# Optimization experiments

Hardware: AMD Instinct MI355X
Metric: run time of the kernel (lower is better)

Reference implementation:

```python
import jax, jax.numpy as jnp
import numpy as np

B, T, C = 2, 2048, 1024
N_HEAD = 16
BAND_WIDTH = 256

def setup_inputs() -> dict:
    key = jax.random.key(0)
    ks = jax.random.split(key, 5)
    s = 1.0 / np.sqrt(C)
    return {
        "x": jax.random.normal(ks[0], (B, T, C), dtype=jnp.float32),
        "Wq": jax.random.normal(ks[1], (C, C), dtype=jnp.float32) * s,
        "bq": jnp.zeros((C,), dtype=jnp.float32),
        "Wk": jax.random.normal(ks[2], (C, C), dtype=jnp.float32) * s,
        "bk": jnp.zeros((C,), dtype=jnp.float32),
        "Wv": jax.random.normal(ks[3], (C, C), dtype=jnp.float32) * s,
        "bv": jnp.zeros((C,), dtype=jnp.float32),
        "Wp": jax.random.normal(ks[4], (C, C), dtype=jnp.float32) * s,
        "bp": jnp.zeros((C,), dtype=jnp.float32),
    }

def _band_mask(t):
    # allowed: j <= i (causal) and j >= i - band_width (band)
    i = jnp.arange(t)[:, None]
    j = jnp.arange(t)[None, :]
    return (j <= i) & (j >= i - BAND_WIDTH)

def reference(x, Wq, bq, Wk, bk, Wv, bv, Wp, bp):
    b, t, c = x.shape
    hd = c // N_HEAD
    # projections -> [b, h, t, hd]
    def heads(w, bias):
        y = x @ w.T + bias
        return y.reshape(b, t, N_HEAD, hd).transpose(0, 2, 1, 3)
    q = heads(Wq, bq)
    k = heads(Wk, bk)
    v = heads(Wv, bv)
    scale = 1.0 / np.sqrt(hd)
    att = jnp.einsum('bhqd,bhkd->bhqk', q, k) * scale  # [b,h,t,t]
    mask = _band_mask(t)
    att = jnp.where(mask[None, None], att, -jnp.inf)
    att = jax.nn.softmax(att, axis=-1)
    y = jnp.einsum('bhqk,bhkd->bhqd', att, v)
    y = y.transpose(0, 2, 1, 3).reshape(b, t, c)
    return y @ Wp.T + bp
```

## Files before the change

kernel.cpp:

```cpp
#include <hip/hip_runtime.h>


typedef __attribute__((ext_vector_type(8))) short bf16x8;
typedef __attribute__((ext_vector_type(8))) unsigned short u16x8;
typedef __attribute__((ext_vector_type(4))) float f32x4;

__device__ __forceinline__ float bf2f(unsigned short u) {
  union { unsigned u; float f; } x; x.u = ((unsigned)u) << 16; return x.f;
}
__device__ __forceinline__ unsigned short f2bf(float f) {
  union { float f; unsigned u; } x; x.f = f;
  unsigned r = x.u + 0x7FFFu + ((x.u >> 16) & 1u);
  return (unsigned short)(r >> 16);
}

#define GLOAD_LDS16(g, l)                                                     \
  __builtin_amdgcn_global_load_lds(                                           \
      (__attribute__((address_space(1))) void*)(g),                           \
      (__attribute__((address_space(3))) void*)(l), 16, 0, 0)

__global__ void cvt_all(const float* __restrict__ x, const float* __restrict__ Wq,
                        const float* __restrict__ Wk, const float* __restrict__ Wv,
                        const float* __restrict__ Wp, unsigned short* __restrict__ xb,
                        unsigned short* __restrict__ wqkv,
                        unsigned short* __restrict__ wpb) {
  int i = blockIdx.x * 256 + threadIdx.x;
  const float* src;
  unsigned short* dst;
  int off;
  if (i < 1048576)      { src = x;  dst = xb;             off = i; }
  else if (i < 1310720) { src = Wq; dst = wqkv;           off = i - 1048576; }
  else if (i < 1572864) { src = Wk; dst = wqkv + 1048576; off = i - 1310720; }
  else if (i < 1835008) { src = Wv; dst = wqkv + 2097152; off = i - 1572864; }
  else                  { src = Wp; dst = wpb;            off = i - 1835008; }
  float4 v = ((const float4*)src)[off];
  ushort4 o;
  o.x = f2bf(v.x); o.y = f2bf(v.y); o.z = f2bf(v.z); o.w = f2bf(v.w);
  ((ushort4*)dst)[off] = o;
}

__global__ __launch_bounds__(256) void gemm_qkv(
    const unsigned short* __restrict__ A, const unsigned short* __restrict__ Wall,
    const float* __restrict__ b0, const float* __restrict__ b1,
    const float* __restrict__ b2, unsigned short* __restrict__ outp) {
  constexpr int K = 1024;
  __shared__ __align__(16) unsigned short As[128 * 32];
  __shared__ __align__(16) unsigned short Bs[128 * 32];
  int tid = threadIdx.x;
  int m0 = blockIdx.x * 128;
  int proj = blockIdx.y >> 3;
  int n0 = (blockIdx.y & 7) * 128;
  const unsigned short* W = Wall + (size_t)proj * (K * 1024);
  const float* bias = (proj == 0) ? b0 : ((proj == 1) ? b1 : b2);
  unsigned short* out = outp + (size_t)proj * 4194304;
  int w = tid >> 6, lane = tid & 63;
  int wm = (w >> 1) * 64, wn = (w & 1) * 64;
  int lm = lane & 15, quad = lane >> 4;

  f32x4 acc[4][4];
#pragma unroll
  for (int mi = 0; mi < 4; ++mi)
#pragma unroll
    for (int ni = 0; ni < 4; ++ni) acc[mi][ni] = (f32x4){0.f, 0.f, 0.f, 0.f};

  int o0 = tid * 16, o1 = o0 + 4096;
  int r0 = o0 >> 6, cb0 = o0 & 63;
  int r1 = o1 >> 6, cb1 = o1 & 63;
  const char* a0 = (const char*)A + (size_t)(m0 + r0) * (K * 2) + cb0;
  const char* a1 = (const char*)A + (size_t)(m0 + r1) * (K * 2) + cb1;
  const char* w0 = (const char*)W + (size_t)(n0 + r0) * (K * 2) + cb0;
  const char* w1 = (const char*)W + (size_t)(n0 + r1) * (K * 2) + cb1;
  char* lA = (char*)As;
  char* lB = (char*)Bs;

  for (int k0 = 0; k0 < K; k0 += 32) {
    GLOAD_LDS16(a0 + k0 * 2, lA + o0);
    GLOAD_LDS16(a1 + k0 * 2, lA + o1);
    GLOAD_LDS16(w0 + k0 * 2, lB + o0);
    GLOAD_LDS16(w1 + k0 * 2, lB + o1);
    __syncthreads();
    bf16x8 af[4], bfv[4];
#pragma unroll
    for (int mi = 0; mi < 4; ++mi)
      af[mi] = *(const bf16x8*)(As + (wm + mi * 16 + lm) * 32 + quad * 8);
#pragma unroll
    for (int ni = 0; ni < 4; ++ni)
      bfv[ni] = *(const bf16x8*)(Bs + (wn + ni * 16 + lm) * 32 + quad * 8);
#pragma unroll
    for (int mi = 0; mi < 4; ++mi)
#pragma unroll
      for (int ni = 0; ni < 4; ++ni)
        acc[mi][ni] = __builtin_amdgcn_mfma_f32_16x16x32_bf16(
            af[mi], bfv[ni], acc[mi][ni], 0, 0, 0);
    __syncthreads();
  }
#pragma unroll
  for (int mi = 0; mi < 4; ++mi) {
#pragma unroll
    for (int ni = 0; ni < 4; ++ni) {
      int gn = n0 + wn + ni * 16 + lm;
      float bv = bias[gn];
#pragma unroll
      for (int r = 0; r < 4; ++r) {
        int gm = m0 + wm + mi * 16 + quad * 4 + r;
        float val = acc[mi][ni][r] + bv;
        int bb = gm >> 11, tt = gm & 2047;
        int hh = gn >> 6, dd = gn & 63;
        size_t idx;
        if (proj == 2)
          idx = (((size_t)bb * 16 + hh) * 64 + dd) * 2048 + tt;
        else
          idx = (((size_t)bb * 16 + hh) * 2048 + tt) * 64 + dd;
        out[idx] = f2bf(val);
      }
    }
  }
}

__global__ __launch_bounds__(256) void gemm_p64(
    const unsigned short* __restrict__ A, const unsigned short* __restrict__ W,
    const float* __restrict__ bias, float* __restrict__ out) {
  constexpr int K = 1024;
  __shared__ __align__(16) unsigned short As[64 * 32];
  __shared__ __align__(16) unsigned short Bs[128 * 32];
  int tid = threadIdx.x;
  int m0 = blockIdx.x * 64, n0 = blockIdx.y * 128;
  int w = tid >> 6, lane = tid & 63;
  int wm = (w >> 1) * 32, wn = (w & 1) * 64;
  int lm = lane & 15, quad = lane >> 4;

  f32x4 acc[2][4];
#pragma unroll
  for (int mi = 0; mi < 2; ++mi)
#pragma unroll
    for (int ni = 0; ni < 4; ++ni) acc[mi][ni] = (f32x4){0.f, 0.f, 0.f, 0.f};

  int o0 = tid * 16, o1 = o0 + 4096;
  int r0 = o0 >> 6, cb0 = o0 & 63;
  int r1 = o1 >> 6, cb1 = o1 & 63;
  const char* ag = (const char*)A + (size_t)(m0 + r0) * (K * 2) + cb0;
  const char* w0 = (const char*)W + (size_t)(n0 + r0) * (K * 2) + cb0;
  const char* w1 = (const char*)W + (size_t)(n0 + r1) * (K * 2) + cb1;
  char* lA = (char*)As;
  char* lB = (char*)Bs;

  for (int k0 = 0; k0 < K; k0 += 32) {
    GLOAD_LDS16(ag + k0 * 2, lA + o0);
    GLOAD_LDS16(w0 + k0 * 2, lB + o0);
    GLOAD_LDS16(w1 + k0 * 2, lB + o1);
    __syncthreads();
    bf16x8 af[2], bfv[4];
#pragma unroll
    for (int mi = 0; mi < 2; ++mi)
      af[mi] = *(const bf16x8*)(As + (wm + mi * 16 + lm) * 32 + quad * 8);
#pragma unroll
    for (int ni = 0; ni < 4; ++ni)
      bfv[ni] = *(const bf16x8*)(Bs + (wn + ni * 16 + lm) * 32 + quad * 8);
#pragma unroll
    for (int mi = 0; mi < 2; ++mi)
#pragma unroll
      for (int ni = 0; ni < 4; ++ni)
        acc[mi][ni] = __builtin_amdgcn_mfma_f32_16x16x32_bf16(
            af[mi], bfv[ni], acc[mi][ni], 0, 0, 0);
    __syncthreads();
  }
#pragma unroll
  for (int mi = 0; mi < 2; ++mi) {
#pragma unroll
    for (int ni = 0; ni < 4; ++ni) {
      int gn = n0 + wn + ni * 16 + lm;
      float bv = bias[gn];
#pragma unroll
      for (int r = 0; r < 4; ++r) {
        int gm = m0 + wm + mi * 16 + quad * 4 + r;
        out[(size_t)gm * 1024 + gn] = acc[mi][ni][r] + bv;
      }
    }
  }
}

__global__ __launch_bounds__(256) void attn_band_mfma(
    const unsigned short* __restrict__ qb, const unsigned short* __restrict__ kb,
    const unsigned short* __restrict__ vtg, unsigned short* __restrict__ yb) {
  __shared__ __align__(16) unsigned short Kb[2][64 * 72];
  __shared__ __align__(16) unsigned short Vb[2][64 * 72];
  int bid = blockIdx.x;
  int qt = bid & 31, h = (bid >> 5) & 15, b = bid >> 9;
  int q0b = qt * 64;
  int tid = threadIdx.x;
  int lane = tid & 63;
  int w = tid >> 6;
  int m = lane & 15, quad = lane >> 4;
  int wq = w * 16;
  int tq0 = q0b + wq;
  size_t hb = ((size_t)(b * 16 + h)) * (2048 * 64);
  size_t vhb = ((size_t)(b * 16 + h)) * (64 * 2048);
  const char* kgb = (const char*)(kb + hb);
  const char* vgb = (const char*)(vtg + vhb);

  int sA = tid, sB = tid + 256, sC = 512 + (tid & 63);
  int rA = sA / 9, kA = sA - rA * 9;
  int rB = sB / 9, kB = sB - rB * 9;
  int rC = sC / 9, kC = sC - rC * 9;
  int okA = (kA < 8) ? kA : 0, okB = (kB < 8) ? kB : 0, okC = (kC < 8) ? kC : 0;
  int offKA = rA * 128 + okA * 16, offVA = rA * 4096 + okA * 16;
  int offKB = rB * 128 + okB * 16, offVB = rB * 4096 + okB * 16;
  int offKC = rC * 128 + okC * 16, offVC = rC * 4096 + okC * 16;

  int jlo = q0b - 256;
  if (jlo < 0) jlo = 0;

  {
    const char* kg = kgb + (size_t)jlo * 128;
    const char* vg = vgb + (size_t)jlo * 2;
    char* kd = (char*)Kb[0];
    char* vd = (char*)Vb[0];
    GLOAD_LDS16(kg + offKA, kd + sA * 16);
    GLOAD_LDS16(kg + offKB, kd + sB * 16);
    GLOAD_LDS16(vg + offVA, vd + sA * 16);
    GLOAD_LDS16(vg + offVB, vd + sB * 16);
    if (tid < 128) {
      const char* g = (tid < 64) ? (kg + offKC) : (vg + offVC);
      char* l = ((tid < 64) ? kd : vd) + sC * 16;
      GLOAD_LDS16(g, l);
    }
  }

  const unsigned short* qrow = qb + hb + (size_t)(tq0 + m) * 64;
  bf16x8 af0 = *(const bf16x8*)(qrow + quad * 8);
  bf16x8 af1 = *(const bf16x8*)(qrow + 32 + quad * 8);

  f32x4 oacc[4];
#pragma unroll
  for (int di = 0; di < 4; ++di) oacc[di] = (f32x4){0.f, 0.f, 0.f, 0.f};
  float lpart[4] = {0.f, 0.f, 0.f, 0.f};

  int cur = 0;
  for (int c0 = jlo; c0 <= q0b; c0 += 64, cur ^= 1) {
    __syncthreads();
    const unsigned short* Kc = Kb[cur];
    const unsigned short* Vc = Vb[cur];
    f32x4 sacc[4];
#pragma unroll
    for (int ni = 0; ni < 4; ++ni) sacc[ni] = (f32x4){0.f, 0.f, 0.f, 0.f};
#pragma unroll
    for (int ni = 0; ni < 4; ++ni) {
      bf16x8 k0 = *(const bf16x8*)(Kc + (ni * 16 + m) * 72 + quad * 8);
      bf16x8 k1 = *(const bf16x8*)(Kc + (ni * 16 + m) * 72 + 32 + quad * 8);
      sacc[ni] = __builtin_amdgcn_mfma_f32_16x16x32_bf16(af0, k0, sacc[ni], 0, 0, 0);
      sacc[ni] = __builtin_amdgcn_mfma_f32_16x16x32_bf16(af1, k1, sacc[ni], 0, 0, 0);
    }
    __syncthreads();
    if (c0 < q0b) {
      const char* kg = kgb + (size_t)(c0 + 64) * 128;
      const char* vg = vgb + (size_t)(c0 + 64) * 2;
      char* kd = (char*)Kb[cur ^ 1];
      char* vd = (char*)Vb[cur ^ 1];
      GLOAD_LDS16(kg + offKA, kd + sA * 16);
      GLOAD_LDS16(kg + offKB, kd + sB * 16);
      GLOAD_LDS16(vg + offVA, vd + sA * 16);
      GLOAD_LDS16(vg + offVB, vd + sB * 16);
      if (tid < 128) {
        const char* g = (tid < 64) ? (kg + offKC) : (vg + offVC);
        char* l = ((tid < 64) ? kd : vd) + sC * 16;
        GLOAD_LDS16(g, l);
      }
    }
    unsigned short* Pw = (unsigned short*)Kc;
#pragma unroll
    for (int ni = 0; ni < 4; ++ni) {
      int j = c0 + ni * 16 + m;
#pragma unroll
      for (int r = 0; r < 4; ++r) {
        int t = tq0 + quad * 4 + r;
        float e = __expf(sacc[ni][r] * 0.125f);
        e = ((unsigned)(t - j) <= 256u) ? e : 0.f;
        lpart[r] += e;
        Pw[(wq + quad * 4 + r) * 72 + ni * 16 + m] = f2bf(e);
      }
    }
#pragma unroll
    for (int ks = 0; ks < 2; ++ks) {
      bf16x8 a = *(const bf16x8*)(Pw + (wq + m) * 72 + ks * 32 + quad * 8);
#pragma unroll
      for (int di = 0; di < 4; ++di) {
        bf16x8 vfr = *(const bf16x8*)(Vc + (di * 16 + m) * 72 + ks * 32 + quad * 8);
        oacc[di] = __builtin_amdgcn_mfma_f32_16x16x32_bf16(a, vfr, oacc[di], 0, 0, 0);
      }
    }
  }
#pragma unroll
  for (int mask = 1; mask <= 8; mask <<= 1)
#pragma unroll
    for (int r = 0; r < 4; ++r) lpart[r] += __shfl_xor(lpart[r], mask, 64);
  float inv[4];
#pragma unroll
  for (int r = 0; r < 4; ++r) inv[r] = 1.f / lpart[r];
  unsigned short* R = &Kb[0][0];
#pragma unroll
  for (int di = 0; di < 4; ++di)
#pragma unroll
    for (int r = 0; r < 4; ++r)
      R[(wq + quad * 4 + r) * 72 + di * 16 + m] = f2bf(oacc[di][r] * inv[r]);
  size_t orow = (size_t)b * 2048 + tq0;
#pragma unroll
  for (int v2 = 0; v2 < 2; ++v2) {
    int v = v2 * 64 + lane;
    int q = v >> 3, dg = v & 7;
    u16x8 val = *(const u16x8*)(R + (wq + q) * 72 + dg * 8);
    *(u16x8*)(yb + (orow + q) * 1024 + h * 64 + dg * 8) = val;
  }
}

extern "C" void kernel_launch(void* const* d_in, const int* in_sizes, int n_in,
                              void* d_out, int out_size, void* d_ws,
                              size_t ws_size, hipStream_t stream) {
  const float* x  = (const float*)d_in[0];
  const float* Wq = (const float*)d_in[1];
  const float* bq = (const float*)d_in[2];
  const float* Wk = (const float*)d_in[3];
  const float* bk = (const float*)d_in[4];
  const float* Wv = (const float*)d_in[5];
  const float* bv = (const float*)d_in[6];
  const float* Wp = (const float*)d_in[7];
  const float* bp = (const float*)d_in[8];
  float* out = (float*)d_out;

  char* ws = (char*)d_ws;
  unsigned short* xb   = (unsigned short*)(ws);
  unsigned short* wqkv = (unsigned short*)(ws + (8ull << 20));
  unsigned short* wpb  = (unsigned short*)(ws + (14ull << 20));
  unsigned short* qkv  = (unsigned short*)(ws + (16ull << 20));
  unsigned short* yb   = (unsigned short*)(ws + (40ull << 20));

  cvt_all<<<8192, 256, 0, stream>>>(x, Wq, Wk, Wv, Wp, xb, wqkv, wpb);
  gemm_qkv<<<dim3(32, 24), 256, 0, stream>>>(xb, wqkv, bq, bk, bv, qkv);
  attn_band_mfma<<<1024, 256, 0, stream>>>(qkv, qkv + 4194304ull,
                                           qkv + 8388608ull, yb);
  gemm_p64<<<dim3(64, 8), 256, 0, stream>>>(yb, wpb, bp, out);
}
```

Baseline: 166.7 us.

## Double attention query tile to 128 rows per block to reuse K/V tiles

Each attention block now handles 128 query rows instead of 64, and each wave computes two 16-row tiles, so every K/V chunk loaded into LDS serves twice as many queries. The key range per block grows by one chunk (6 instead of 5 for full bands), which cuts redundant K/V traffic across overlapping bands. An extra LDS buffer holds P and the output for the upper waves. The cost is half as many blocks (512), more registers per wave and more LDS per block, which may reduce occupancy and leave fewer blocks per CU.

```diff
diff --git a/kernel.cpp b/kernel.cpp
--- a/kernel.cpp
+++ b/kernel.cpp
@@ -184,14 +184,15 @@
     const unsigned short* __restrict__ vtg, unsigned short* __restrict__ yb) {
   __shared__ __align__(16) unsigned short Kb[2][64 * 72];
   __shared__ __align__(16) unsigned short Vb[2][64 * 72];
+  __shared__ __align__(16) unsigned short Pe[64 * 72];
   int bid = blockIdx.x;
-  int qt = bid & 31, h = (bid >> 5) & 15, b = bid >> 9;
-  int q0b = qt * 64;
+  int qt = bid & 15, h = (bid >> 4) & 15, b = bid >> 8;
+  int q0b = qt * 128;
   int tid = threadIdx.x;
   int lane = tid & 63;
   int w = tid >> 6;
   int m = lane & 15, quad = lane >> 4;
-  int wq = w * 16;
+  int wq = w * 32;
   int tq0 = q0b + wq;
   size_t hb = ((size_t)(b * 16 + h)) * (2048 * 64);
   size_t vhb = ((size_t)(b * 16 + h)) * (64 * 2048);
@@ -209,6 +210,7 @@
 
   int jlo = q0b - 256;
   if (jlo < 0) jlo = 0;
+  int cend = q0b + 64;
 
   {
     const char* kg = kgb + (size_t)jlo * 128;
@@ -226,32 +228,45 @@
     }
   }
 
-  const unsigned short* qrow = qb + hb + (size_t)(tq0 + m) * 64;
-  bf16x8 af0 = *(const bf16x8*)(qrow + quad * 8);
-  bf16x8 af1 = *(const bf16x8*)(qrow + 32 + quad * 8);
-
-  f32x4 oacc[4];
-#pragma unroll
-  for (int di = 0; di < 4; ++di) oacc[di] = (f32x4){0.f, 0.f, 0.f, 0.f};
-  float lpart[4] = {0.f, 0.f, 0.f, 0.f};
+  bf16x8 af[2][2];
+#pragma unroll
+  for (int mt = 0; mt < 2; ++mt) {
+    const unsigned short* qrow = qb + hb + (size_t)(tq0 + mt * 16 + m) * 64;
+    af[mt][0] = *(const bf16x8*)(qrow + quad * 8);
+    af[mt][1] = *(const bf16x8*)(qrow + 32 + quad * 8);
+  }
+
+  f32x4 oacc[2][4];
+#pragma unroll
+  for (int mt = 0; mt < 2; ++mt)
+#pragma unroll
+    for (int di = 0; di < 4; ++di) oacc[mt][di] = (f32x4){0.f, 0.f, 0.f, 0.f};
+  float lpart[2][4] = {{0.f, 0.f, 0.f, 0.f}, {0.f, 0.f, 0.f, 0.f}};
 
   int cur = 0;
-  for (int c0 = jlo; c0 <= q0b; c0 += 64, cur ^= 1) {
+  for (int c0 = jlo; c0 <= cend; c0 += 64, cur ^= 1) {
     __syncthreads();
     const unsigned short* Kc = Kb[cur];
     const unsigned short* Vc = Vb[cur];
-    f32x4 sacc[4];
-#pragma unroll
-    for (int ni = 0; ni < 4; ++ni) sacc[ni] = (f32x4){0.f, 0.f, 0.f, 0.f};
+    f32x4 sacc[2][4];
+#pragma unroll
+    for (int mt = 0; mt < 2; ++mt)
+#pragma unroll
+      for (int ni = 0; ni < 4; ++ni) sacc[mt][ni] = (f32x4){0.f, 0.f, 0.f, 0.f};
 #pragma unroll
     for (int ni = 0; ni < 4; ++ni) {
       bf16x8 k0 = *(const bf16x8*)(Kc + (ni * 16 + m) * 72 + quad * 8);
       bf16x8 k1 = *(const bf16x8*)(Kc + (ni * 16 + m) * 72 + 32 + quad * 8);
-      sacc[ni] = __builtin_amdgcn_mfma_f32_16x16x32_bf16(af0, k0, sacc[ni], 0, 0, 0);
-      sacc[ni] = __builtin_amdgcn_mfma_f32_16x16x32_bf16(af1, k1, sacc[ni], 0, 0, 0);
-    }
-    __syncthreads();
-    if (c0 < q0b) {
+#pragma unroll
+      for (int mt = 0; mt < 2; ++mt) {
+        sacc[mt][ni] =
+            __builtin_amdgcn_mfma_f32_16x16x32_bf16(af[mt][0], k0, sacc[mt][ni], 0, 0, 0);
+        sacc[mt][ni] =
+            __builtin_amdgcn_mfma_f32_16x16x32_bf16(af[mt][1], k1, sacc[mt][ni], 0, 0, 0);
+      }
+    }
+    __syncthreads();
+    if (c0 < cend) {
       const char* kg = kgb + (size_t)(c0 + 64) * 128;
       const char* vg = vgb + (size_t)(c0 + 64) * 2;
       char* kd = (char*)Kb[cur ^ 1];
@@ -266,48 +281,67 @@
         GLOAD_LDS16(g, l);
       }
     }
-    unsigned short* Pw = (unsigned short*)Kc;
-#pragma unroll
-    for (int ni = 0; ni < 4; ++ni) {
-      int j = c0 + ni * 16 + m;
-#pragma unroll
-      for (int r = 0; r < 4; ++r) {
-        int t = tq0 + quad * 4 + r;
-        float e = __expf(sacc[ni][r] * 0.125f);
-        e = ((unsigned)(t - j) <= 256u) ? e : 0.f;
-        lpart[r] += e;
-        Pw[(wq + quad * 4 + r) * 72 + ni * 16 + m] = f2bf(e);
+    unsigned short* Pbase =
+        (w < 2) ? (unsigned short*)Kc : (unsigned short*)Pe;
+    int prow0 = (w < 2) ? wq : (wq - 64);
+#pragma unroll
+    for (int mt = 0; mt < 2; ++mt) {
+#pragma unroll
+      for (int ni = 0; ni < 4; ++ni) {
+        int j = c0 + ni * 16 + m;
+#pragma unroll
+        for (int r = 0; r < 4; ++r) {
+          int t = tq0 + mt * 16 + quad * 4 + r;
+          float e = __expf(sacc[mt][ni][r] * 0.125f);
+          e = ((unsigned)(t - j) <= 256u) ? e : 0.f;
+          lpart[mt][r] += e;
+          Pbase[(prow0 + mt * 16 + quad * 4 + r) * 72 + ni * 16 + m] = f2bf(e);
+        }
       }
     }
 #pragma unroll
     for (int ks = 0; ks < 2; ++ks) {
-      bf16x8 a = *(const bf16x8*)(Pw + (wq + m) * 72 + ks * 32 + quad * 8);
+      bf16x8 a0 = *(const bf16x8*)(Pbase + (prow0 + m) * 72 + ks * 32 + quad * 8);
+      bf16x8 a1 =
+          *(const bf16x8*)(Pbase + (prow0 + 16 + m) * 72 + ks * 32 + quad * 8);
 #pragma unroll
       for (int di = 0; di < 4; ++di) {
         bf16x8 vfr = *(const bf16x8*)(Vc + (di * 16 + m) * 72 + ks * 32 + quad * 8);
-        oacc[di] = __builtin_amdgcn_mfma_f32_16x16x32_bf16(a, vfr, oacc[di], 0, 0, 0);
+        oacc[0][di] = __builtin_amdgcn_mfma_f32_16x16x32_bf16(a0, vfr, oacc[0][di], 0, 0, 0);
+        oacc[1][di] = __builtin_amdgcn_mfma_f32_16x16x32_bf16(a1, vfr, oacc[1][di], 0, 0, 0);
       }
     }
   }
 #pragma unroll
   for (int mask = 1; mask <= 8; mask <<= 1)
 #pragma unroll
-    for (int r = 0; r < 4; ++r) lpart[r] += __shfl_xor(lpart[r], mask, 64);
-  float inv[4];
-#pragma unroll
-  for (int r = 0; r < 4; ++r) inv[r] = 1.f / lpart[r];
-  unsigned short* R = &Kb[0][0];
-#pragma unroll
-  for (int di = 0; di < 4; ++di)
-#pragma unroll
-    for (int r = 0; r < 4; ++r)
-      R[(wq + quad * 4 + r) * 72 + di * 16 + m] = f2bf(oacc[di][r] * inv[r]);
-  size_t orow = (size_t)b * 2048 + tq0;
-#pragma unroll
-  for (int v2 = 0; v2 < 2; ++v2) {
-    int v = v2 * 64 + lane;
+    for (int mt = 0; mt < 2; ++mt)
+#pragma unroll
+      for (int r = 0; r < 4; ++r) lpart[mt][r] += __shfl_xor(lpart[mt][r], mask, 64);
+  float inv[2][4];
+#pragma unroll
+  for (int mt = 0; mt < 2; ++mt)
+#pragma unroll
+    for (int r = 0; r < 4; ++r) inv[mt][r] = 1.f / lpart[mt][r];
+  unsigned short* Rbase = (w < 2) ? (unsigned short*)Kb[0] : (unsigned short*)Pe;
+  int rrow0 = (w < 2) ? wq : (wq - 64);
+#pragma unroll
+  for (int mt = 0; mt < 2; ++mt)
+#pragma unroll
+    for (int di = 0; di < 4; ++di)
+#pragma unroll
+      for (int r = 0; r < 4; ++r)
+        Rbase[(rrow0 + mt * 16 + quad * 4 + r) * 72 + di * 16 + m] =
+            f2bf(oacc[mt][di][r] * inv[mt][r]);
+  __syncthreads();
+  size_t orow = (size_t)b * 2048 + q0b;
+#pragma unroll
+  for (int it = 0; it < 4; ++it) {
+    int v = it * 256 + tid;
     int q = v >> 3, dg = v & 7;
-    u16x8 val = *(const u16x8*)(R + (wq + q) * 72 + dg * 8);
+    const unsigned short* src =
+        (q < 64) ? (const unsigned short*)Kb[0] : (const unsigned short*)Pe;
+    u16x8 val = *(const u16x8*)(src + (q & 63) * 72 + dg * 8);
     *(u16x8*)(yb + (orow + q) * 1024 + h * 64 + dg * 8) = val;
   }
 }
@@ -335,7 +369,7 @@
 
   cvt_all<<<8192, 256, 0, stream>>>(x, Wq, Wk, Wv, Wp, xb, wqkv, wpb);
   gemm_qkv<<<dim3(32, 24), 256, 0, stream>>>(xb, wqkv, bq, bk, bv, qkv);
-  attn_band_mfma<<<1024, 256, 0, stream>>>(qkv, qkv + 4194304ull,
-                                           qkv + 8388608ull, yb);
+  attn_band_mfma<<<512, 256, 0, stream>>>(qkv, qkv + 4194304ull,
+                                          qkv + 8388608ull, yb);
   gemm_p64<<<dim3(64, 8), 256, 0, stream>>>(yb, wpb, bp, out);
 }
```

After: 167.7 us. About the same (+0.6%).
